# Kernel tuning notes

Hardware: AMD Instinct MI355X
Metric: run time of the kernel (lower is better)

The kernel has to match this reference:

```python
import jax, jax.numpy as jnp
import numpy as np

D_MODEL = 1024
NUM_HEADS = 16
HEAD_DIM = D_MODEL // NUM_HEADS
WINDOW = 64
GLOBAL_TOKENS = 4
MAX_SEQ_LEN = 2048
RANDOM_TOKENS = 32
BATCH = 2
SEQ = 2048
NEG = -1.0e9
LN_EPS = 1e-5


def setup_inputs() -> dict:
    key = jax.random.key(0)
    k1, k2, k3, k4 = jax.random.split(key, 4)
    x = jax.random.normal(k1, (BATCH, SEQ, D_MODEL), dtype=jnp.float32)
    w_qkv = jax.random.normal(k2, (D_MODEL, 3 * D_MODEL), dtype=jnp.float32) * (D_MODEL ** -0.5)
    w_out = jax.random.normal(k3, (D_MODEL, D_MODEL), dtype=jnp.float32) * (D_MODEL ** -0.5)
    ln_gamma = jnp.ones((D_MODEL,), dtype=jnp.float32)
    ln_beta = jnp.zeros((D_MODEL,), dtype=jnp.float32)
    rand_idx = jax.random.randint(k4, (MAX_SEQ_LEN, RANDOM_TOKENS), 0, MAX_SEQ_LEN, dtype=jnp.int32)
    return {"x": x, "w_qkv": w_qkv, "w_out": w_out,
            "ln_gamma": ln_gamma, "ln_beta": ln_beta, "rand_idx": rand_idx}


def _build_masks(seq_len, rand_idx):
    i = jnp.arange(seq_len)
    causal = (i[:, None] >= i[None, :]).astype(jnp.float32)  # [L,L], lower-triangular
    # local window mask
    dist = jnp.abs(i[:, None] - i[None, :])
    local = (dist <= WINDOW).astype(jnp.float32) * causal
    # global column mask: columns {0..G-1} u {L-G..L-1}, rows i >= g (== causal on those cols)
    gcols = jnp.concatenate([jnp.arange(GLOBAL_TOKENS), jnp.arange(seq_len - GLOBAL_TOKENS, seq_len)])
    is_gcol = jnp.zeros((seq_len,), jnp.float32).at[gcols].set(1.0)
    glob = is_gcol[None, :] * causal
    # random mask: per-row fixed random columns, then causal-filtered
    ri = rand_idx[:seq_len]  # [L, R]
    rows = jnp.broadcast_to(i[:, None], ri.shape)
    rnd = jnp.zeros((seq_len, seq_len), jnp.float32).at[rows, ri].set(1.0) * causal
    return local, glob, rnd


def reference(x, w_qkv, w_out, ln_gamma, ln_beta, rand_idx):
    B, L, _ = x.shape
    residual = x
    # LayerNorm
    mu = jnp.mean(x, axis=-1, keepdims=True)
    var = jnp.mean(jnp.square(x - mu), axis=-1, keepdims=True)
    xn = (x - mu) * jax.lax.rsqrt(var + LN_EPS) * ln_gamma + ln_beta
    # QKV projection
    qkv = xn @ w_qkv
    q, k, v = jnp.split(qkv, 3, axis=-1)
    q = q.reshape(B, L, NUM_HEADS, HEAD_DIM).transpose(0, 2, 1, 3)  # [B,H,L,D]
    k = k.reshape(B, L, NUM_HEADS, HEAD_DIM).transpose(0, 2, 1, 3)
    v = v.reshape(B, L, NUM_HEADS, HEAD_DIM).transpose(0, 2, 1, 3)
    local, glob, rnd = _build_masks(L, rand_idx)
    raw = jnp.einsum('bhqd,bhkd->bhqk', q, k) / jnp.sqrt(jnp.float32(HEAD_DIM))
    # original sums three masked copies of the same scores:
    # combined = 3*raw + ((1-local)+(1-glob)+(1-rnd)) * NEG
    penalty = (3.0 - (local + glob + rnd)) * NEG  # [L,L]
    combined = 3.0 * raw + penalty[None, None, :, :]
    attn = jax.nn.softmax(combined, axis=-1)
    out = jnp.einsum('bhqk,bhkd->bhqd', attn, v)
    out = out.transpose(0, 2, 1, 3).reshape(B, L, D_MODEL)
    out = out @ w_out
    return out + residual
```

## Files before the change

### kernel.cpp

```cpp
#include <hip/hip_runtime.h>
#include <stdint.h>

typedef __attribute__((ext_vector_type(8))) short shortx8;
typedef __attribute__((ext_vector_type(4))) float floatx4;

static constexpr int SEQ_    = 2048;
static constexpr int DMODEL  = 1024;
static constexpr int HDIM    = 64;
static constexpr int BATCH_  = 2;
static constexpr int NHEADS  = 16;
static constexpr int WINDOW_ = 64;
static constexpr int GTOK    = 4;
static constexpr int RTOK    = 32;
static constexpr int ROWS    = BATCH_ * SEQ_;
static constexpr int QKVN    = 3 * DMODEL;

__device__ inline unsigned short f2bf(float f) {
  union { float f; unsigned int u; } x; x.f = f;
  unsigned int r = (x.u + 0x7FFFu + ((x.u >> 16) & 1u)) >> 16;
  return (unsigned short)r;
}
__device__ inline float bf2f(unsigned short b) {
  union { unsigned int u; float f; } x; x.u = ((unsigned int)b) << 16;
  return x.f;
}

__device__ inline void gload_lds16(const void* g, void* l) {
  __builtin_amdgcn_global_load_lds(
      (const __attribute__((address_space(1))) void*)g,
      (__attribute__((address_space(3))) void*)l, 16, 0, 0);
}

__device__ __forceinline__ void gemm_core_k1024(
    const unsigned short* __restrict__ aSrc0, const unsigned short* __restrict__ aSrc1,
    const unsigned short* __restrict__ bSrc,
    unsigned short* Al, unsigned short* Bl,
    const int wave, const int lane, floatx4 (&acc)[4][2]) {
  const int quad = lane >> 4, l16 = lane & 15;
  const int wm = (wave >> 1) * 64, wn = (wave & 1) * 32;
  unsigned short* AlD0 = Al + (wave * 32) * 32;
  unsigned short* AlD1 = Al + (wave * 32 + 16) * 32;
  unsigned short* BlD  = Bl + (wave * 16) * 32;
  for (int k0 = 0; k0 < 1024; k0 += 32) {
    __syncthreads();
    gload_lds16(aSrc0 + k0, AlD0);
    gload_lds16(aSrc1 + k0, AlD1);
    gload_lds16(bSrc  + k0, BlD);
    __syncthreads();
    shortx8 af[4], bfr[2];
    #pragma unroll
    for (int s = 0; s < 4; s++)
      af[s] = *(const shortx8*)&Al[(wm + s * 16 + l16) * 32 + quad * 8];
    #pragma unroll
    for (int s = 0; s < 2; s++)
      bfr[s] = *(const shortx8*)&Bl[(wn + s * 16 + l16) * 32 + quad * 8];
    #pragma unroll
    for (int sm = 0; sm < 4; sm++)
      #pragma unroll
      for (int sn = 0; sn < 2; sn++)
        acc[sm][sn] = __builtin_amdgcn_mfma_f32_16x16x32_bf16(af[sm], bfr[sn], acc[sm][sn], 0, 0, 0);
  }
}

__global__ __launch_bounds__(256) void k1_prep(
    const float* __restrict__ x, const float* __restrict__ w_qkv,
    const float* __restrict__ w_out, const float* __restrict__ gamma,
    const float* __restrict__ beta, const int* __restrict__ ridx,
    unsigned short* __restrict__ xn, unsigned short* __restrict__ wqT,
    unsigned short* __restrict__ woT, unsigned short* __restrict__ Wvs,
    int* __restrict__ cols, int* __restrict__ cnt, int* __restrict__ tmx,
    int* __restrict__ qlist) {
  __shared__ float tile[32][33];
  __shared__ float red[4], red2[4];
  __shared__ int rl[RTOK];
  __shared__ int scount, stm;
  const int bx = blockIdx.x;
  const int t = threadIdx.x;
  if (bx < 3072) {
    int n0 = (bx % 96) * 32, k0 = (bx / 96) * 32;
    int tx = t & 31, ty = t >> 5;
    #pragma unroll
    for (int r = ty; r < 32; r += 8)
      tile[r][tx] = w_qkv[(size_t)(k0 + r) * QKVN + n0 + tx];
    __syncthreads();
    #pragma unroll
    for (int r = ty; r < 32; r += 8)
      wqT[(size_t)(n0 + r) * DMODEL + k0 + tx] = f2bf(tile[tx][r]);
  } else if (bx < 7168) {
    int row = bx - 3072;
    const float4* xr = (const float4*)(x + (size_t)row * DMODEL);
    float4 v = xr[t];
    float s = v.x + v.y + v.z + v.w;
    #pragma unroll
    for (int o = 32; o > 0; o >>= 1) s += __shfl_xor(s, o);
    int wave = t >> 6, lane = t & 63;
    if (lane == 0) red[wave] = s;
    __syncthreads();
    float mean = (red[0] + red[1] + red[2] + red[3]) * (1.0f / DMODEL);
    float dx = v.x - mean, dy = v.y - mean, dz = v.z - mean, dw = v.w - mean;
    float q = dx*dx + dy*dy + dz*dz + dw*dw;
    #pragma unroll
    for (int o = 32; o > 0; o >>= 1) q += __shfl_xor(q, o);
    if (lane == 0) red2[wave] = q;
    __syncthreads();
    float var = (red2[0] + red2[1] + red2[2] + red2[3]) * (1.0f / DMODEL);
    float rs = rsqrtf(var + 1e-5f);
    float4 g = ((const float4*)gamma)[t];
    float4 bb = ((const float4*)beta)[t];
    ushort4 outv;
    outv.x = f2bf(dx * rs * g.x + bb.x);
    outv.y = f2bf(dy * rs * g.y + bb.y);
    outv.z = f2bf(dz * rs * g.z + bb.z);
    outv.w = f2bf(dw * rs * g.w + bb.w);
    ((ushort4*)(xn + (size_t)row * DMODEL))[t] = outv;
  } else if (bx < 8192) {
    int idx = bx - 7168;
    int n0 = (idx & 31) * 32, k0 = (idx >> 5) * 32;
    int tx = t & 31, ty = t >> 5;
    #pragma unroll
    for (int r = ty; r < 32; r += 8)
      tile[r][tx] = w_out[(size_t)(k0 + r) * DMODEL + n0 + tx];
    __syncthreads();
    #pragma unroll
    for (int r = ty; r < 32; r += 8)
      woT[(size_t)(n0 + r) * DMODEL + k0 + tx] = f2bf(tile[tx][r]);
  } else if (bx < 9216) {
    int idx = bx - 8192;
    int v0 = (idx & 31) * 32, k0 = (idx >> 5) * 32;
    int tx = t & 31, ty = t >> 5;
    #pragma unroll
    for (int r = ty; r < 32; r += 8)
      Wvs[(size_t)(k0 + r) * DMODEL + v0 + tx] =
          f2bf(w_qkv[(size_t)(k0 + r) * QKVN + 2 * DMODEL + v0 + tx]);
  } else {
    const int i = bx - 9216;
    if (t < RTOK) rl[t] = ridx[i * RTOK + t];
    if (t == 0) { scount = 0; stm = 0; }
    __syncthreads();
    const int wstart = (i - WINDOW_ > 0) ? (i - WINDOW_) : 0;
    const int c = t;
    int j = -1;
    bool valid = false;
    if (c < 65) {
      j = i - WINDOW_ + c;
      valid = (j >= 0);
    } else if (c < 73) {
      int g = c - 65;
      j = (g < 4) ? g : (SEQ_ - 8 + g);
      valid = (j <= i) && (j < wstart);
    } else if (c < 73 + RTOK) {
      int r = c - 73;
      j = rl[r];
      bool dup = false;
      for (int r2 = 0; r2 < r; r2++) dup = dup || (rl[r2] == j);
      valid = (j <= i) && (j < wstart) && !(j < GTOK || j >= SEQ_ - GTOK) && !dup;
    }
    int tier = -1;
    if (valid) {
      int loc = ((i - j) <= WINDOW_) ? 1 : 0;
      int glb = (j < GTOK || j >= SEQ_ - GTOK) ? 1 : 0;
      int rnd = 0;
      for (int r = 0; r < RTOK; r++) rnd |= (rl[r] == j) ? 1 : 0;
      tier = loc + glb + rnd;
      atomicMax(&stm, tier);
    }
    __syncthreads();
    const int tm = stm;
    if (valid && tier == tm) {
      int pos = atomicAdd(&scount, 1);
      cols[i * 128 + pos] = j;
    }
    __syncthreads();
    if (t == 0) {
      cnt[i] = scount;
      tmx[i] = tm;
      if (i < 68 || i >= SEQ_ - 4) {
        int cc = (i < 68) ? i : 68 + (i - (SEQ_ - 4));
        qlist[cc * 2 + 0] = (tm == 3) ? i : -1;
        qlist[cc * 2 + 1] = (tm == 3) ? (SEQ_ + i) : -1;
      }
    }
  }
}

__global__ __launch_bounds__(256) void k2_wgemm(
    const unsigned short* __restrict__ woT, const unsigned short* __restrict__ Wvs,
    unsigned short* __restrict__ WvoT, const unsigned short* __restrict__ xn,
    const unsigned short* __restrict__ wqT, const int* __restrict__ qlist,
    unsigned short* __restrict__ qf, unsigned short* __restrict__ kf,
    unsigned short* __restrict__ vf) {
  __shared__ unsigned short Al[128 * 32];
  __shared__ unsigned short Bl[64 * 32];
  const int bx = blockIdx.x, t = threadIdx.x;
  const int wave = t >> 6, lane = t & 63;
  const int lrow = lane >> 2, lkoff = (lane & 3) * 8;
  const int quad = lane >> 4, l16 = lane & 15;
  const int wm = (wave >> 1) * 64, wn = (wave & 1) * 32;
  floatx4 acc[4][2] = {};
  if (bx < 128) {
    const int bm = (bx >> 4) * 128, bn = (bx & 15) * 64;
    const unsigned short* a0 = woT + (size_t)(bm + wave * 32 + lrow) * DMODEL + lkoff;
    const unsigned short* a1 = a0 + 16 * DMODEL;
    const unsigned short* b0 = Wvs + (size_t)(bn + wave * 16 + lrow) * DMODEL + lkoff;
    gemm_core_k1024(a0, a1, b0, Al, Bl, wave, lane, acc);
    #pragma unroll
    for (int sm = 0; sm < 4; sm++)
      #pragma unroll
      for (int sn = 0; sn < 2; sn++)
        #pragma unroll
        for (int r = 0; r < 4; r++) {
          int row = bm + wm + sm * 16 + quad * 4 + r;
          int col = bn + wn + sn * 16 + l16;
          WvoT[(size_t)row * DMODEL + col] = f2bf(acc[sm][sn][r]);
        }
  } else {
    const int idx = bx - 128;
    const int job = idx >> 4, bn = (idx & 15) * 64;
    const int wsel = (job < 2) ? 0 : ((job == 2) ? 1 : 2);
    const unsigned short* BT = wqT + (size_t)wsel * DMODEL * DMODEL;
    unsigned short* dstbuf = (job == 0) ? qf
                           : (job == 1) ? (qf + (size_t)128 * DMODEL)
                           : (job == 2) ? kf : vf;
    int rsrc[2];
    #pragma unroll
    for (int q = 0; q < 2; q++) {
      int m = wave * 32 + q * 16 + lrow;
      int row;
      if (job < 2) {
        int s = job * 128 + m;
        int ql = (s < 144) ? qlist[s] : -1;
        row = (ql < 0) ? 0 : ql;
      } else {
        row = (m < 16) ? ((m >> 3) * SEQ_ + (((m & 7) < 4) ? (m & 7) : (SEQ_ - 8 + (m & 7)))) : 0;
      }
      rsrc[q] = row;
    }
    const unsigned short* a0 = xn + (size_t)rsrc[0] * DMODEL + lkoff;
    const unsigned short* a1 = xn + (size_t)rsrc[1] * DMODEL + lkoff;
    const unsigned short* b0 = BT + (size_t)(bn + wave * 16 + lrow) * DMODEL + lkoff;
    gemm_core_k1024(a0, a1, b0, Al, Bl, wave, lane, acc);
    #pragma unroll
    for (int sm = 0; sm < 4; sm++)
      #pragma unroll
      for (int sn = 0; sn < 2; sn++)
        #pragma unroll
        for (int r = 0; r < 4; r++) {
          int m = wm + sm * 16 + quad * 4 + r;
          int col = bn + wn + sn * 16 + l16;
          dstbuf[(size_t)m * DMODEL + col] = f2bf(acc[sm][sn][r]);
        }
  }
}

__global__ __launch_bounds__(256) void k3_xbar(
    const unsigned short* __restrict__ xn, const int* __restrict__ cols,
    const int* __restrict__ cnt, const int* __restrict__ tmx,
    const int* __restrict__ qlist, const unsigned short* __restrict__ qf,
    const unsigned short* __restrict__ kf, const unsigned short* __restrict__ vf,
    unsigned short* __restrict__ xbar, unsigned short* __restrict__ vbar) {
  const int bx = blockIdx.x, t = threadIdx.x;
  const int wave = t >> 6, lane = t & 63;
  if (bx < 1024) {
    __shared__ unsigned short win[80][256];
    const int b = bx >> 9, rest = bx & 511;
    const int i0 = (rest >> 2) * 16, dimbase = (rest & 3) * 256;
    const size_t xnb = (size_t)(b * SEQ_) * DMODEL;
    const int lo = i0 - 64;
    #pragma unroll 4
    for (int it = 0; it < 20; it++) {
      int r = it * 4 + wave;
      int gr = lo + r;
      if (gr >= 0)
        *(ushort4*)&win[r][lane * 4] =
            *(const ushort4*)(xn + xnb + (size_t)gr * DMODEL + dimbase + lane * 4);
    }
    __syncthreads();
    const unsigned short* xnd = xn + xnb + dimbase + lane * 4;
    for (int rr = 0; rr < 4; rr++) {
      const int i = i0 + wave * 4 + rr;
      const int tm = tmx[i], n = cnt[i];
      ushort4 o;
      if (tm == 3) {
        o.x = o.y = o.z = o.w = 0;
      } else {
        int jr0 = cols[i * 128 + lane];
        int jr1 = cols[i * 128 + 64 + lane];
        float4 s0 = {0,0,0,0}, s1 = {0,0,0,0}, s2 = {0,0,0,0}, s3 = {0,0,0,0};
        auto ldcol = [&](int j) -> ushort4 {
          if (j >= lo) return *(const ushort4*)&win[j - lo][lane * 4];
          return *(const ushort4*)(xnd + (size_t)j * DMODEL);
        };
        auto acc4 = [](float4& s, ushort4 v) {
          s.x += bf2f(v.x); s.y += bf2f(v.y); s.z += bf2f(v.z); s.w += bf2f(v.w);
        };
        const int nA = (n < 64) ? n : 64;
        int c = 0;
        for (; c + 4 <= nA; c += 4) {
          int j0 = __shfl(jr0, c), j1 = __shfl(jr0, c + 1);
          int j2 = __shfl(jr0, c + 2), j3 = __shfl(jr0, c + 3);
          ushort4 v0 = ldcol(j0), v1 = ldcol(j1), v2 = ldcol(j2), v3 = ldcol(j3);
          acc4(s0, v0); acc4(s1, v1); acc4(s2, v2); acc4(s3, v3);
        }
        for (; c < nA; c++) acc4(s0, ldcol(__shfl(jr0, c)));
        c = 64;
        for (; c + 4 <= n; c += 4) {
          int j0 = __shfl(jr1, c - 64), j1 = __shfl(jr1, c - 63);
          int j2 = __shfl(jr1, c - 62), j3 = __shfl(jr1, c - 61);
          ushort4 v0 = ldcol(j0), v1 = ldcol(j1), v2 = ldcol(j2), v3 = ldcol(j3);
          acc4(s0, v0); acc4(s1, v1); acc4(s2, v2); acc4(s3, v3);
        }
        for (; c < n; c++) acc4(s0, ldcol(__shfl(jr1, c - 64)));
        float inv = 1.0f / (float)n;
        o.x = f2bf((s0.x + s1.x + s2.x + s3.x) * inv);
        o.y = f2bf((s0.y + s1.y + s2.y + s3.y) * inv);
        o.z = f2bf((s0.z + s1.z + s2.z + s3.z) * inv);
        o.w = f2bf((s0.w + s1.w + s2.w + s3.w) * inv);
      }
      *(ushort4*)(xbar + (size_t)(b * SEQ_ + i) * DMODEL + dimbase + lane * 4) = o;
    }
  } else {
    const int s = (bx - 1024) * 4 + wave;
    const int dst = (s < 144) ? qlist[s] : -1;
    if (dst < 0) return;
    const int b = dst >> 11, i = dst & (SEQ_ - 1);
    const int n = cnt[i];
    int myk = 0;
    if (lane < n) {
      int kj = cols[i * 128 + lane];
      myk = b * 8 + ((kj < 4) ? kj : (kj - (SEQ_ - 8)));
    }
    for (int h = 0; h < NHEADS; h++) {
      float qd = bf2f(qf[(size_t)s * DMODEL + h * HDIM + lane]);
      float w[8];
      float m = -1e30f;
      for (int c = 0; c < n; c++) {
        int ks = __shfl(myk, c);
        float kd = bf2f(kf[(size_t)ks * DMODEL + h * HDIM + lane]);
        float p = qd * kd;
        #pragma unroll
        for (int o = 32; o > 0; o >>= 1) p += __shfl_xor(p, o);
        p *= 0.375f;
        w[c] = p;
        m = fmaxf(m, p);
      }
      float denom = 0.f, acc = 0.f;
      for (int c = 0; c < n; c++) {
        int ks = __shfl(myk, c);
        float e = __expf(w[c] - m);
        denom += e;
        acc += e * bf2f(vf[(size_t)ks * DMODEL + h * HDIM + lane]);
      }
      vbar[(size_t)s * DMODEL + h * HDIM + lane] = f2bf(acc / denom);
    }
  }
}

__global__ __launch_bounds__(256) void k4_final(
    const unsigned short* __restrict__ xbar, const unsigned short* __restrict__ WvoT,
    const unsigned short* __restrict__ vbar, const unsigned short* __restrict__ woT,
    const int* __restrict__ qlist, const int* __restrict__ tmx,
    const float* __restrict__ x, float* __restrict__ out) {
  __shared__ unsigned short Al[128 * 32];
  __shared__ unsigned short Bl[64 * 32];
  __shared__ int rowinf[128];
  const int bx = blockIdx.x, t = threadIdx.x;
  const int wave = t >> 6, lane = t & 63;
  const int lrow = lane >> 2, lkoff = (lane & 3) * 8;
  const int quad = lane >> 4, l16 = lane & 15;
  const int wm = (wave >> 1) * 64, wn = (wave & 1) * 32;
  floatx4 acc[4][2] = {};
  if (bx < 512) {
    const int bm = (bx >> 4) * 128, bn = (bx & 15) * 64;
    if (t < 128) rowinf[t] = tmx[(bm + t) & (SEQ_ - 1)];
    const unsigned short* a0 = xbar + (size_t)(bm + wave * 32 + lrow) * DMODEL + lkoff;
    const unsigned short* a1 = a0 + 16 * DMODEL;
    const unsigned short* b0 = WvoT + (size_t)(bn + wave * 16 + lrow) * DMODEL + lkoff;
    gemm_core_k1024(a0, a1, b0, Al, Bl, wave, lane, acc);
    #pragma unroll
    for (int sm = 0; sm < 4; sm++)
      #pragma unroll
      for (int sn = 0; sn < 2; sn++)
        #pragma unroll
        for (int r = 0; r < 4; r++) {
          int m = wm + sm * 16 + quad * 4 + r;
          if (rowinf[m] != 3) {
            int col = bn + wn + sn * 16 + l16;
            size_t off = (size_t)(bm + m) * DMODEL + col;
            out[off] = acc[sm][sn][r] + x[off];
          }
        }
  } else {
    const int idx = bx - 512;
    const int bm = (idx >> 4) * 128, bn = (idx & 15) * 64;
    if (t < 128) {
      int s = bm + t;
      rowinf[t] = (s < 144) ? qlist[s] : -1;
    }
    const unsigned short* a0 = vbar + (size_t)(bm + wave * 32 + lrow) * DMODEL + lkoff;
    const unsigned short* a1 = a0 + 16 * DMODEL;
    const unsigned short* b0 = woT + (size_t)(bn + wave * 16 + lrow) * DMODEL + lkoff;
    gemm_core_k1024(a0, a1, b0, Al, Bl, wave, lane, acc);
    #pragma unroll
    for (int sm = 0; sm < 4; sm++)
      #pragma unroll
      for (int sn = 0; sn < 2; sn++)
        #pragma unroll
        for (int r = 0; r < 4; r++) {
          int m = wm + sm * 16 + quad * 4 + r;
          int dst = rowinf[m];
          if (dst >= 0) {
            int col = bn + wn + sn * 16 + l16;
            size_t off = (size_t)dst * DMODEL + col;
            out[off] = acc[sm][sn][r] + x[off];
          }
        }
  }
}

extern "C" void kernel_launch(void* const* d_in, const int* in_sizes, int n_in,
                              void* d_out, int out_size, void* d_ws, size_t ws_size,
                              hipStream_t stream) {
  const float* x     = (const float*)d_in[0];
  const float* w_qkv = (const float*)d_in[1];
  const float* w_out = (const float*)d_in[2];
  const float* gamma = (const float*)d_in[3];
  const float* beta  = (const float*)d_in[4];
  const int*   ridx  = (const int*)d_in[5];
  float* out = (float*)d_out;

  char* ws = (char*)d_ws;
  size_t off = 0;
  auto alloc = [&](size_t bytes) {
    char* p = ws + off;
    off = (off + bytes + 255) & ~(size_t)255;
    return p;
  };
  unsigned short* xn   = (unsigned short*)alloc((size_t)ROWS * DMODEL * 2);
  unsigned short* wqT  = (unsigned short*)alloc((size_t)QKVN * DMODEL * 2);
  unsigned short* woT  = (unsigned short*)alloc((size_t)DMODEL * DMODEL * 2);
  unsigned short* Wvs  = (unsigned short*)alloc((size_t)DMODEL * DMODEL * 2);
  unsigned short* WvoT = (unsigned short*)alloc((size_t)DMODEL * DMODEL * 2);
  unsigned short* xbar = (unsigned short*)alloc((size_t)ROWS * DMODEL * 2);
  unsigned short* qf   = (unsigned short*)alloc((size_t)256 * DMODEL * 2);
  unsigned short* kf   = (unsigned short*)alloc((size_t)128 * DMODEL * 2);
  unsigned short* vf   = (unsigned short*)alloc((size_t)128 * DMODEL * 2);
  unsigned short* vbar = (unsigned short*)alloc((size_t)256 * DMODEL * 2);
  int* cols  = (int*)alloc((size_t)SEQ_ * 128 * 4);
  int* cnt   = (int*)alloc((size_t)SEQ_ * 4);
  int* tmx   = (int*)alloc((size_t)SEQ_ * 4);
  int* qlist = (int*)alloc(256 * 4);

  hipLaunchKernelGGL(k1_prep, dim3(11264), dim3(256), 0, stream,
                     x, w_qkv, w_out, gamma, beta, ridx,
                     xn, wqT, woT, Wvs, cols, cnt, tmx, qlist);
  hipLaunchKernelGGL(k2_wgemm, dim3(192), dim3(256), 0, stream,
                     woT, Wvs, WvoT, xn, wqT, qlist, qf, kf, vf);
  hipLaunchKernelGGL(k3_xbar, dim3(1060), dim3(256), 0, stream,
                     xn, cols, cnt, tmx, qlist, qf, kf, vf, xbar, vbar);
  hipLaunchKernelGGL(k4_final, dim3(544), dim3(256), 0, stream,
                     xbar, WvoT, vbar, woT, qlist, tmx, x, out);
}
```

Baseline: 186.7 us.

## Use sliding-window running sum for xbar window columns in k3

k1 now writes the window columns at the front of each row's column list and the non-window columns at the back, and records both counts packed into a new array. For rows whose max tier is 1 (window plus extras), k3 keeps a running sum over the 65-row causal window, updated by adding one row and subtracting one row per step. Only the few non-window columns are then gathered, instead of re-summing all 65 window rows per query row. The shared-memory tile load is also widened to 16-byte accesses. The running sum adds float add/subtract drift and gives a slower, non-unrolled path for other tiers.

```diff
diff --git a/kernel.cpp b/kernel.cpp
--- a/kernel.cpp
+++ b/kernel.cpp
@@ -69,11 +69,11 @@
     unsigned short* __restrict__ xn, unsigned short* __restrict__ wqT,
     unsigned short* __restrict__ woT, unsigned short* __restrict__ Wvs,
     int* __restrict__ cols, int* __restrict__ cnt, int* __restrict__ tmx,
-    int* __restrict__ qlist) {
+    int* __restrict__ cnts2, int* __restrict__ qlist) {
   __shared__ float tile[32][33];
   __shared__ float red[4], red2[4];
   __shared__ int rl[RTOK];
-  __shared__ int scount, stm;
+  __shared__ int scw, scnw, stm;
   const int bx = blockIdx.x;
   const int t = threadIdx.x;
   if (bx < 3072) {
@@ -135,12 +135,13 @@
   } else {
     const int i = bx - 9216;
     if (t < RTOK) rl[t] = ridx[i * RTOK + t];
-    if (t == 0) { scount = 0; stm = 0; }
+    if (t == 0) { scw = 0; scnw = 0; stm = 0; }
     __syncthreads();
     const int wstart = (i - WINDOW_ > 0) ? (i - WINDOW_) : 0;
     const int c = t;
     int j = -1;
     bool valid = false;
+    bool iswin = (c < 65);
     if (c < 65) {
       j = i - WINDOW_ + c;
       valid = (j >= 0);
@@ -167,13 +168,19 @@
     __syncthreads();
     const int tm = stm;
     if (valid && tier == tm) {
-      int pos = atomicAdd(&scount, 1);
-      cols[i * 128 + pos] = j;
+      if (iswin) {
+        int pos = atomicAdd(&scw, 1);
+        cols[i * 128 + pos] = j;
+      } else {
+        int pos = 127 - atomicAdd(&scnw, 1);
+        cols[i * 128 + pos] = j;
+      }
     }
     __syncthreads();
     if (t == 0) {
-      cnt[i] = scount;
+      cnt[i] = scw + scnw;
       tmx[i] = tm;
+      cnts2[i] = scw | (scnw << 16);
       if (i < 68 || i >= SEQ_ - 4) {
         int cc = (i < 68) ? i : 68 + (i - (SEQ_ - 4));
         qlist[cc * 2 + 0] = (tm == 3) ? i : -1;
@@ -255,8 +262,9 @@
 __global__ __launch_bounds__(256) void k3_xbar(
     const unsigned short* __restrict__ xn, const int* __restrict__ cols,
     const int* __restrict__ cnt, const int* __restrict__ tmx,
-    const int* __restrict__ qlist, const unsigned short* __restrict__ qf,
-    const unsigned short* __restrict__ kf, const unsigned short* __restrict__ vf,
+    const int* __restrict__ cnts2, const int* __restrict__ qlist,
+    const unsigned short* __restrict__ qf, const unsigned short* __restrict__ kf,
+    const unsigned short* __restrict__ vf,
     unsigned short* __restrict__ xbar, unsigned short* __restrict__ vbar) {
   const int bx = blockIdx.x, t = threadIdx.x;
   const int wave = t >> 6, lane = t & 63;
@@ -266,55 +274,91 @@
     const int i0 = (rest >> 2) * 16, dimbase = (rest & 3) * 256;
     const size_t xnb = (size_t)(b * SEQ_) * DMODEL;
     const int lo = i0 - 64;
-    #pragma unroll 4
-    for (int it = 0; it < 20; it++) {
-      int r = it * 4 + wave;
-      int gr = lo + r;
-      if (gr >= 0)
-        *(ushort4*)&win[r][lane * 4] =
-            *(const ushort4*)(xn + xnb + (size_t)gr * DMODEL + dimbase + lane * 4);
+    {
+      const int l5 = lane & 31, rsub = lane >> 5;
+      #pragma unroll 5
+      for (int it = 0; it < 10; it++) {
+        int r = it * 8 + wave * 2 + rsub;
+        int gr = lo + r;
+        if (gr >= 0)
+          *(int4*)&win[r][l5 * 8] =
+              *(const int4*)(xn + xnb + (size_t)gr * DMODEL + dimbase + l5 * 8);
+      }
     }
     __syncthreads();
     const unsigned short* xnd = xn + xnb + dimbase + lane * 4;
+    auto ldcol = [&](int j) -> ushort4 {
+      if (j >= lo) return *(const ushort4*)&win[j - lo][lane * 4];
+      return *(const ushort4*)(xnd + (size_t)j * DMODEL);
+    };
+    auto add4 = [](float4& s, ushort4 v) {
+      s.x += bf2f(v.x); s.y += bf2f(v.y); s.z += bf2f(v.z); s.w += bf2f(v.w);
+    };
+    auto sub4 = [](float4& s, ushort4 v) {
+      s.x -= bf2f(v.x); s.y -= bf2f(v.y); s.z -= bf2f(v.z); s.w -= bf2f(v.w);
+    };
+    const int r0 = i0 + wave * 4;
+    float4 ws = {0, 0, 0, 0};
+    {
+      float4 t1 = {0,0,0,0}, t2 = {0,0,0,0}, t3 = {0,0,0,0};
+      const int jstart = (r0 - 64 > 0) ? (r0 - 64) : 0;
+      const int cn = r0 - jstart + 1;
+      const int base = jstart - lo;
+      int c = 0;
+      for (; c + 4 <= cn; c += 4) {
+        ushort4 v0 = *(const ushort4*)&win[base + c][lane * 4];
+        ushort4 v1 = *(const ushort4*)&win[base + c + 1][lane * 4];
+        ushort4 v2 = *(const ushort4*)&win[base + c + 2][lane * 4];
+        ushort4 v3 = *(const ushort4*)&win[base + c + 3][lane * 4];
+        add4(ws, v0); add4(t1, v1); add4(t2, v2); add4(t3, v3);
+      }
+      for (; c < cn; c++) add4(ws, *(const ushort4*)&win[base + c][lane * 4]);
+      ws.x += t1.x + t2.x + t3.x; ws.y += t1.y + t2.y + t3.y;
+      ws.z += t1.z + t2.z + t3.z; ws.w += t1.w + t2.w + t3.w;
+    }
     for (int rr = 0; rr < 4; rr++) {
-      const int i = i0 + wave * 4 + rr;
-      const int tm = tmx[i], n = cnt[i];
+      const int i = r0 + rr;
+      if (rr > 0) {
+        add4(ws, *(const ushort4*)&win[i - lo][lane * 4]);
+        int dj = i - 65;
+        if (dj >= 0) sub4(ws, *(const ushort4*)&win[dj - lo][lane * 4]);
+      }
+      const int tm = tmx[i];
       ushort4 o;
       if (tm == 3) {
         o.x = o.y = o.z = o.w = 0;
       } else {
-        int jr0 = cols[i * 128 + lane];
-        int jr1 = cols[i * 128 + 64 + lane];
-        float4 s0 = {0,0,0,0}, s1 = {0,0,0,0}, s2 = {0,0,0,0}, s3 = {0,0,0,0};
-        auto ldcol = [&](int j) -> ushort4 {
-          if (j >= lo) return *(const ushort4*)&win[j - lo][lane * 4];
-          return *(const ushort4*)(xnd + (size_t)j * DMODEL);
-        };
-        auto acc4 = [](float4& s, ushort4 v) {
-          s.x += bf2f(v.x); s.y += bf2f(v.y); s.z += bf2f(v.z); s.w += bf2f(v.w);
-        };
-        const int nA = (n < 64) ? n : 64;
-        int c = 0;
-        for (; c + 4 <= nA; c += 4) {
-          int j0 = __shfl(jr0, c), j1 = __shfl(jr0, c + 1);
-          int j2 = __shfl(jr0, c + 2), j3 = __shfl(jr0, c + 3);
-          ushort4 v0 = ldcol(j0), v1 = ldcol(j1), v2 = ldcol(j2), v3 = ldcol(j3);
-          acc4(s0, v0); acc4(s1, v1); acc4(s2, v2); acc4(s3, v3);
+        const int c2 = cnts2[i];
+        const int cw = c2 & 0xffff, cnw = c2 >> 16;
+        const int jr1 = cols[i * 128 + 64 + lane];
+        float4 s;
+        if (tm == 1) {
+          s = ws;
+          float4 t1 = {0,0,0,0}, t2 = {0,0,0,0}, t3 = {0,0,0,0};
+          const int bb = 64 - cnw;
+          int c = 0;
+          for (; c + 4 <= cnw; c += 4) {
+            int j0 = __shfl(jr1, bb + c),     j1 = __shfl(jr1, bb + c + 1);
+            int j2 = __shfl(jr1, bb + c + 2), j3 = __shfl(jr1, bb + c + 3);
+            ushort4 v0 = ldcol(j0), v1 = ldcol(j1), v2 = ldcol(j2), v3 = ldcol(j3);
+            add4(s, v0); add4(t1, v1); add4(t2, v2); add4(t3, v3);
+          }
+          for (; c < cnw; c++) add4(s, ldcol(__shfl(jr1, bb + c)));
+          s.x += t1.x + t2.x + t3.x; s.y += t1.y + t2.y + t3.y;
+          s.z += t1.z + t2.z + t3.z; s.w += t1.w + t2.w + t3.w;
+        } else {
+          const int jr0 = cols[i * 128 + lane];
+          s.x = s.y = s.z = s.w = 0.f;
+          for (int c = 0; c < cw; c++) {
+            int j = (c < 64) ? __shfl(jr0, c) : __shfl(jr1, c - 64);
+            add4(s, ldcol(j));
+          }
+          const int bb = 64 - cnw;
+          for (int c = 0; c < cnw; c++) add4(s, ldcol(__shfl(jr1, bb + c)));
         }
-        for (; c < nA; c++) acc4(s0, ldcol(__shfl(jr0, c)));
-        c = 64;
-        for (; c + 4 <= n; c += 4) {
-          int j0 = __shfl(jr1, c - 64), j1 = __shfl(jr1, c - 63);
-          int j2 = __shfl(jr1, c - 62), j3 = __shfl(jr1, c - 61);
-          ushort4 v0 = ldcol(j0), v1 = ldcol(j1), v2 = ldcol(j2), v3 = ldcol(j3);
-          acc4(s0, v0); acc4(s1, v1); acc4(s2, v2); acc4(s3, v3);
-        }
-        for (; c < n; c++) acc4(s0, ldcol(__shfl(jr1, c - 64)));
-        float inv = 1.0f / (float)n;
-        o.x = f2bf((s0.x + s1.x + s2.x + s3.x) * inv);
-        o.y = f2bf((s0.y + s1.y + s2.y + s3.y) * inv);
-        o.z = f2bf((s0.z + s1.z + s2.z + s3.z) * inv);
-        o.w = f2bf((s0.w + s1.w + s2.w + s3.w) * inv);
+        const float inv = 1.0f / (float)(cw + cnw);
+        o.x = f2bf(s.x * inv); o.y = f2bf(s.y * inv);
+        o.z = f2bf(s.z * inv); o.w = f2bf(s.w * inv);
       }
       *(ushort4*)(xbar + (size_t)(b * SEQ_ + i) * DMODEL + dimbase + lane * 4) = o;
     }
@@ -448,15 +492,16 @@
   int* cols  = (int*)alloc((size_t)SEQ_ * 128 * 4);
   int* cnt   = (int*)alloc((size_t)SEQ_ * 4);
   int* tmx   = (int*)alloc((size_t)SEQ_ * 4);
+  int* cnts2 = (int*)alloc((size_t)SEQ_ * 4);
   int* qlist = (int*)alloc(256 * 4);
 
   hipLaunchKernelGGL(k1_prep, dim3(11264), dim3(256), 0, stream,
                      x, w_qkv, w_out, gamma, beta, ridx,
-                     xn, wqT, woT, Wvs, cols, cnt, tmx, qlist);
+                     xn, wqT, woT, Wvs, cols, cnt, tmx, cnts2, qlist);
   hipLaunchKernelGGL(k2_wgemm, dim3(192), dim3(256), 0, stream,
                      woT, Wvs, WvoT, xn, wqT, qlist, qf, kf, vf);
   hipLaunchKernelGGL(k3_xbar, dim3(1060), dim3(256), 0, stream,
-                     xn, cols, cnt, tmx, qlist, qf, kf, vf, xbar, vbar);
+                     xn, cols, cnt, tmx, cnts2, qlist, qf, kf, vf, xbar, vbar);
   hipLaunchKernelGGL(k4_final, dim3(544), dim3(256), 0, stream,
                      xbar, WvoT, vbar, woT, qlist, tmx, x, out);
 }
```

Measured after the change: 174.5 us. 6.5% less time.
